# Kernel tuning notes

Measured on AMD Instinct MI355X. Metric: run time of the kernel, lower is better.

Reference implementation:

```python
import jax, jax.numpy as jnp
import numpy as np

DT = 0.001          # time step
P = 2               # geomloss p -> cost = ||x-y||^2 / 2, eps = blur**p
BLUR = 0.01
SCALING = 0.5       # eps annealing ratio per step is SCALING**P
SPARSE = 1          # sparse_sampling
N_STEPS = 24        # fixed annealing+refinement iteration count (jit-static)


def setup_inputs() -> dict:
    key = jax.random.key(0)
    k1, k2 = jax.random.split(key)
    B, S, NT, NR = 2, 4, 256, 64
    syn_data = jax.random.normal(k1, (B, S, NT, NR), jnp.float32)
    obs_data = jax.random.normal(k2, (B, S, NT, NR), jnp.float32)
    return {"syn_data": syn_data, "obs_data": obs_data}


def _softmin(eps, C, h):
    # h: [m] = log-weights + potential/eps ; C: [n, m]
    return -eps * jax.nn.logsumexp(h[None, :] - C / eps, axis=1)


def _pairwise_cost(a, b):
    # geomloss p=2 cost: squared euclidean distance / 2
    return 0.5 * jnp.sum((a[:, None, :] - b[None, :, :]) ** 2, axis=-1)


def _sinkhorn_divergence(x, y):
    # x, y: [n, 2] point clouds with uniform weights 1/n.
    # Debiased Sinkhorn divergence S = OT_eps(x,y) - 0.5 OT(x,x) - 0.5 OT(y,y)
    # computed via log-domain iterations with epsilon annealing from
    # diameter**p down to blur**p (ratio scaling**p), as in geomloss.
    n = x.shape[0]
    la = jnp.full((n,), -np.log(n), x.dtype)  # log uniform weights
    Cxy = _pairwise_cost(x, y)
    Cyx = Cxy.T
    Cxx = _pairwise_cost(x, x)
    Cyy = _pairwise_cost(y, y)

    xy = jnp.concatenate([x, y], axis=0)
    diameter = jnp.max(jnp.max(xy, axis=0) - jnp.min(xy, axis=0))
    eps0 = diameter ** P
    eps_min = jnp.asarray(BLUR ** P, x.dtype)
    ratio = SCALING ** P
    eps_list = jnp.maximum(eps0 * ratio ** jnp.arange(N_STEPS, dtype=x.dtype), eps_min)

    zeros = jnp.zeros((n,), x.dtype)

    def step(carry, eps):
        f, g, px, py = carry
        f_new = _softmin(eps, Cxy, la + g / eps)
        g_new = _softmin(eps, Cyx, la + f / eps)
        # symmetric (debiasing) potentials use damped fixed-point updates
        px_new = 0.5 * (px + _softmin(eps, Cxx, la + px / eps))
        py_new = 0.5 * (py + _softmin(eps, Cyy, la + py / eps))
        return (f_new, g_new, px_new, py_new), None

    (f, g, px, py), _ = jax.lax.scan(step, (zeros, zeros, zeros, zeros), eps_list)
    w = jnp.exp(la)  # uniform 1/n
    return jnp.sum(w * (f - px)) + jnp.sum(w * (g - py))


def reference(syn_data, obs_data):
    B, S, NT, NR = syn_data.shape
    # trace mask: drop receiver only if BOTH obs and syn traces are all-zero
    mask1 = jnp.sum(jnp.abs(obs_data), axis=2) == 0  # [B,S,NR]
    mask2 = jnp.sum(jnp.abs(syn_data), axis=2) == 0
    mask = ~(mask1 & mask2)

    t = jnp.arange(NT, dtype=syn_data.dtype)[::SPARSE] * DT  # [NTs]
    obs_tr = jnp.swapaxes(obs_data[:, :, ::SPARSE, :], 2, 3)  # [B,S,NR,NTs]
    syn_tr = jnp.swapaxes(syn_data[:, :, ::SPARSE, :], 2, 3)
    tb = jnp.broadcast_to(t, obs_tr.shape)
    obs_pts = jnp.stack([tb, obs_tr], axis=-1)  # [B,S,NR,NTs,2]
    syn_pts = jnp.stack([tb, syn_tr], axis=-1)

    nts = obs_pts.shape[3]
    flat_obs = obs_pts.reshape(B * S * NR, nts, 2)
    flat_syn = syn_pts.reshape(B * S * NR, nts, 2)
    div = jax.vmap(_sinkhorn_divergence)(flat_obs, flat_syn)  # [B*S*NR]
    div = div.reshape(B, S, NR)
    return jnp.sum(jnp.where(mask, div, jnp.zeros_like(div)), axis=(1, 2))  # [B]
```

## Files before the change

### kernel.cpp

```cpp
#include <hip/hip_runtime.h>


constexpr int   N       = 256;
constexpr int   NPROB   = 512;
constexpr int   NRDIM   = 64;
constexpr float DT_F    = 0.001f;
constexpr float EPS_MIN = 1e-4f;
constexpr int   NSTEPS  = 24;
constexpr float LOG2E   = 1.4426950408889634f;
constexpr float LN2     = 0.6931471805599453f;
constexpr int   NT      = 512;

extern "C" __global__ void __launch_bounds__(NT, 4)
sinkhorn_div_kernel(const float* __restrict__ syn,
                    const float* __restrict__ obs,
                    float* __restrict__ divs)
{
    const int p    = blockIdx.x;
    const int r    = p & (NRDIM - 1);
    const int bs   = p >> 6;
    const int tid  = threadIdx.x;
    const int row  = tid & (N - 1);
    const int pair = tid >> 8;

    __shared__ float4 ya4[2][N];
    __shared__ float4 xa4[2][N];
    __shared__ float  redA[32];

    float* yaF = (float*)ya4;
    float* xaF = (float*)xa4;

    const size_t base = (size_t)bs * N * NRDIM + r;
    const float xi = obs[base + (size_t)row * NRDIM];
    const float yi = syn[base + (size_t)row * NRDIM];
    const float ti = (float)row * DT_F;

    if (pair == 0) {
        const float2 w2 = make_float2(yi, ti);
        *(float2*)&yaF[       row * 4 + 2] = w2;
        *(float2*)&yaF[1024 + row * 4 + 2] = w2;
    } else {
        const float2 w2 = make_float2(xi, ti);
        *(float2*)&xaF[       row * 4 + 2] = w2;
        *(float2*)&xaF[1024 + row * 4 + 2] = w2;
    }

    float hi = fmaxf(xi, yi), lo = fminf(xi, yi);
    float ax = fabsf(xi),     ay = fabsf(yi);
    #pragma unroll
    for (int off = 32; off > 0; off >>= 1) {
        hi  = fmaxf(hi, __shfl_down(hi, off, 64));
        lo  = fminf(lo, __shfl_down(lo, off, 64));
        ax += __shfl_down(ax, off, 64);
        ay += __shfl_down(ay, off, 64);
    }
    const int wave = tid >> 6;
    if ((tid & 63) == 0) {
        redA[wave * 4 + 0] = hi;  redA[wave * 4 + 1] = lo;
        redA[wave * 4 + 2] = ax;  redA[wave * 4 + 3] = ay;
    }
    __syncthreads();
    float vmax = -3.4e38f, vmin = 3.4e38f, sax = 0.0f, say = 0.0f;
    #pragma unroll
    for (int w = 0; w < 8; ++w) {
        vmax = fmaxf(vmax, redA[w * 4 + 0]);
        vmin = fminf(vmin, redA[w * 4 + 1]);
        sax += redA[w * 4 + 2];
        say += redA[w * 4 + 3];
    }

    const float tspread  = 255.0f * DT_F;
    const float diameter = fmaxf(tspread, vmax - vmin);
    float eps_raw = diameter * diameter;

    const float selfx = 0.5f * (ti * ti + xi * xi);
    const float selfy = 0.5f * (ti * ti + yi * yi);
    const float la2   = -8.0f;

    const float self1 = (pair == 0) ? selfx : selfy;
    const float self2 = (pair == 0) ? selfy : selfx;
    const float cf1   = (pair == 0) ? xi : yi;
    const float cf2   = (pair == 0) ? yi : xi;

    float pot1 = 0.0f, pot2 = 0.0f;

#define EXP2(x) __builtin_amdgcn_exp2f(x)

    for (int step = 0; step < NSTEPS; ++step) {
        const float eps = fmaxf(eps_raw, EPS_MIN);
        const float inv = LOG2E / eps;
        const int   bo  = (step & 1) * 1024;

        const float h1 = fmaf(pot1 - self1, inv, la2);
        const float h2 = fmaf(pot2 - self2, inv, la2);
        if (pair == 0) {
            xaF[bo + row * 4 + 0] = h1;
            yaF[bo + row * 4 + 1] = h2;
        } else {
            yaF[bo + row * 4 + 0] = h1;
            xaF[bo + row * 4 + 1] = h2;
        }
        __syncthreads();

        const float tii = ti * inv;
        const float c1  = cf1 * inv;
        const float c2  = cf2 * inv;
        const float4* __restrict__ Hq = (pair == 0) ? &ya4[step & 1][0]
                                                    : &xa4[step & 1][0];

        float m0 = -1e9f, m1 = -1e9f, s0 = 0.0f, s1 = 0.0f;
        #pragma unroll 4
        for (int jb = 0; jb < N; jb += 8) {
            const float4 Q0 = Hq[jb + 0];
            const float4 Q1 = Hq[jb + 1];
            const float4 Q2 = Hq[jb + 2];
            const float4 Q3 = Hq[jb + 3];
            const float4 Q4 = Hq[jb + 4];
            const float4 Q5 = Hq[jb + 5];
            const float4 Q6 = Hq[jb + 6];
            const float4 Q7 = Hq[jb + 7];
            const float b0 = fmaf(c1, Q0.z, fmaf(tii, Q0.w, Q0.x));
            const float c0_ = fmaf(c2, Q0.z, fmaf(tii, Q0.w, Q0.y));
            const float b1 = fmaf(c1, Q1.z, fmaf(tii, Q1.w, Q1.x));
            const float c1_ = fmaf(c2, Q1.z, fmaf(tii, Q1.w, Q1.y));
            const float b2 = fmaf(c1, Q2.z, fmaf(tii, Q2.w, Q2.x));
            const float c2_ = fmaf(c2, Q2.z, fmaf(tii, Q2.w, Q2.y));
            const float b3 = fmaf(c1, Q3.z, fmaf(tii, Q3.w, Q3.x));
            const float c3_ = fmaf(c2, Q3.z, fmaf(tii, Q3.w, Q3.y));
            const float b4 = fmaf(c1, Q4.z, fmaf(tii, Q4.w, Q4.x));
            const float c4_ = fmaf(c2, Q4.z, fmaf(tii, Q4.w, Q4.y));
            const float b5 = fmaf(c1, Q5.z, fmaf(tii, Q5.w, Q5.x));
            const float c5_ = fmaf(c2, Q5.z, fmaf(tii, Q5.w, Q5.y));
            const float b6 = fmaf(c1, Q6.z, fmaf(tii, Q6.w, Q6.x));
            const float c6_ = fmaf(c2, Q6.z, fmaf(tii, Q6.w, Q6.y));
            const float b7 = fmaf(c1, Q7.z, fmaf(tii, Q7.w, Q7.x));
            const float c7_ = fmaf(c2, Q7.z, fmaf(tii, Q7.w, Q7.y));
            const float bt0 = fmaxf(fmaxf(b0, b1), b2);
            const float bt1 = fmaxf(fmaxf(b3, b4), b5);
            const float bt2 = fmaxf(fmaxf(b6, b7), m0);
            const float M0  = ceilf(fmaxf(fmaxf(bt0, bt1), bt2));
            const float ct0 = fmaxf(fmaxf(c0_, c1_), c2_);
            const float ct1 = fmaxf(fmaxf(c3_, c4_), c5_);
            const float ct2 = fmaxf(fmaxf(c6_, c7_), m1);
            const float M1  = ceilf(fmaxf(fmaxf(ct0, ct1), ct2));
            const float t0 =
                ((EXP2(b0 - M0) + EXP2(b1 - M0)) + (EXP2(b2 - M0) + EXP2(b3 - M0))) +
                ((EXP2(b4 - M0) + EXP2(b5 - M0)) + (EXP2(b6 - M0) + EXP2(b7 - M0)));
            const float t1 =
                ((EXP2(c0_ - M1) + EXP2(c1_ - M1)) + (EXP2(c2_ - M1) + EXP2(c3_ - M1))) +
                ((EXP2(c4_ - M1) + EXP2(c5_ - M1)) + (EXP2(c6_ - M1) + EXP2(c7_ - M1)));
            s0 = ldexpf(s0, (int)(m0 - M0)) + t0;  m0 = M0;
            s1 = ldexpf(s1, (int)(m1 - M1)) + t1;  m1 = M1;
        }

        const float el2 = eps * LN2;
        pot1 = self1 - el2 * (m0 + __builtin_amdgcn_logf(s0));
        pot2 = 0.5f * (pot2 + (self2 - el2 * (m1 + __builtin_amdgcn_logf(s1))));

        eps_raw *= 0.25f;
    }
#undef EXP2

    float contrib = pot1 - pot2;
    #pragma unroll
    for (int off = 32; off > 0; off >>= 1)
        contrib += __shfl_down(contrib, off, 64);
    __syncthreads();
    if ((tid & 63) == 0) redA[wave] = contrib;
    __syncthreads();
    if (tid == 0) {
        float total = 0.0f;
        #pragma unroll
        for (int w = 0; w < 8; ++w) total += redA[w];
        total *= (1.0f / (float)N);
        const bool masked_out = (sax == 0.0f) && (say == 0.0f);
        divs[p] = masked_out ? 0.0f : total;
    }
}

extern "C" __global__ void __launch_bounds__(256)
reduce_out_kernel(const float* __restrict__ divs, float* __restrict__ out)
{
    const int b   = blockIdx.x;
    const int tid = threadIdx.x;
    __shared__ float red[4];
    float v = divs[b * 256 + tid];
    #pragma unroll
    for (int off = 32; off > 0; off >>= 1)
        v += __shfl_down(v, off, 64);
    if ((tid & 63) == 0) red[tid >> 6] = v;
    __syncthreads();
    if (tid == 0) out[b] = red[0] + red[1] + red[2] + red[3];
}

extern "C" void kernel_launch(void* const* d_in, const int* in_sizes, int n_in,
                              void* d_out, int out_size, void* d_ws, size_t ws_size,
                              hipStream_t stream) {
    const float* syn = (const float*)d_in[0];
    const float* obs = (const float*)d_in[1];
    float* divs = (float*)d_ws;

    sinkhorn_div_kernel<<<NPROB, NT, 0, stream>>>(syn, obs, divs);
    reduce_out_kernel<<<2, 256, 0, stream>>>(divs, (float*)d_out);
}
```

Measured before the change: 589.3 us.

## Split each row's logsumexp across two half-waves with 1024-thread blocks

Doubles the block to 1024 threads so that two lanes, one in each half of a wave, cover each cost-matrix row. Each lane reduces half of the columns, and the partial (max, sum) pairs are merged with a cross-half shuffle before the potential update. This halves the serial inner-loop length per thread and adds parallelism for 512 blocks on the device. The cost is an extra shuffle-merge every step, a larger per-block footprint (launch bounds now 1024 threads with 8 waves per EU), and duplicated min/max/abs reductions in the redundant half-lanes.

```diff
diff --git a/kernel.cpp b/kernel.cpp
--- a/kernel.cpp
+++ b/kernel.cpp
@@ -9,9 +9,9 @@
 constexpr int   NSTEPS  = 24;
 constexpr float LOG2E   = 1.4426950408889634f;
 constexpr float LN2     = 0.6931471805599453f;
-constexpr int   NT      = 512;
-
-extern "C" __global__ void __launch_bounds__(NT, 4)
+constexpr int   NT      = 1024;
+
+extern "C" __global__ void __launch_bounds__(NT, 8)
 sinkhorn_div_kernel(const float* __restrict__ syn,
                     const float* __restrict__ obs,
                     float* __restrict__ divs)
@@ -20,12 +20,15 @@
     const int r    = p & (NRDIM - 1);
     const int bs   = p >> 6;
     const int tid  = threadIdx.x;
-    const int row  = tid & (N - 1);
-    const int pair = tid >> 8;
+    const int lane = tid & 63;
+    const int wave = tid >> 6;
+    const int pair = tid >> 9;
+    const int half = lane >> 5;
+    const int row  = ((wave & 7) << 5) | (lane & 31);
 
     __shared__ float4 ya4[2][N];
     __shared__ float4 xa4[2][N];
-    __shared__ float  redA[32];
+    __shared__ float  redA[64];
 
     float* yaF = (float*)ya4;
     float* xaF = (float*)xa4;
@@ -35,14 +38,16 @@
     const float yi = syn[base + (size_t)row * NRDIM];
     const float ti = (float)row * DT_F;
 
-    if (pair == 0) {
-        const float2 w2 = make_float2(yi, ti);
-        *(float2*)&yaF[       row * 4 + 2] = w2;
-        *(float2*)&yaF[1024 + row * 4 + 2] = w2;
-    } else {
-        const float2 w2 = make_float2(xi, ti);
-        *(float2*)&xaF[       row * 4 + 2] = w2;
-        *(float2*)&xaF[1024 + row * 4 + 2] = w2;
+    if (half == 0) {
+        if (pair == 0) {
+            const float2 w2 = make_float2(yi, ti);
+            *(float2*)&yaF[       row * 4 + 2] = w2;
+            *(float2*)&yaF[1024 + row * 4 + 2] = w2;
+        } else {
+            const float2 w2 = make_float2(xi, ti);
+            *(float2*)&xaF[       row * 4 + 2] = w2;
+            *(float2*)&xaF[1024 + row * 4 + 2] = w2;
+        }
     }
 
     float hi = fmaxf(xi, yi), lo = fminf(xi, yi);
@@ -54,7 +59,6 @@
         ax += __shfl_down(ax, off, 64);
         ay += __shfl_down(ay, off, 64);
     }
-    const int wave = tid >> 6;
     if ((tid & 63) == 0) {
         redA[wave * 4 + 0] = hi;  redA[wave * 4 + 1] = lo;
         redA[wave * 4 + 2] = ax;  redA[wave * 4 + 3] = ay;
@@ -62,7 +66,7 @@
     __syncthreads();
     float vmax = -3.4e38f, vmin = 3.4e38f, sax = 0.0f, say = 0.0f;
     #pragma unroll
-    for (int w = 0; w < 8; ++w) {
+    for (int w = 0; w < 16; ++w) {
         vmax = fmaxf(vmax, redA[w * 4 + 0]);
         vmin = fminf(vmin, redA[w * 4 + 1]);
         sax += redA[w * 4 + 2];
@@ -84,6 +88,8 @@
 
     float pot1 = 0.0f, pot2 = 0.0f;
 
+    const int jhalf = half << 7;
+
 #define EXP2(x) __builtin_amdgcn_exp2f(x)
 
     for (int step = 0; step < NSTEPS; ++step) {
@@ -91,14 +97,16 @@
         const float inv = LOG2E / eps;
         const int   bo  = (step & 1) * 1024;
 
-        const float h1 = fmaf(pot1 - self1, inv, la2);
-        const float h2 = fmaf(pot2 - self2, inv, la2);
-        if (pair == 0) {
-            xaF[bo + row * 4 + 0] = h1;
-            yaF[bo + row * 4 + 1] = h2;
-        } else {
-            yaF[bo + row * 4 + 0] = h1;
-            xaF[bo + row * 4 + 1] = h2;
+        if (half == 0) {
+            const float h1 = fmaf(pot1 - self1, inv, la2);
+            const float h2 = fmaf(pot2 - self2, inv, la2);
+            if (pair == 0) {
+                xaF[bo + row * 4 + 0] = h1;
+                yaF[bo + row * 4 + 1] = h2;
+            } else {
+                yaF[bo + row * 4 + 0] = h1;
+                xaF[bo + row * 4 + 1] = h2;
+            }
         }
         __syncthreads();
 
@@ -110,7 +118,8 @@
 
         float m0 = -1e9f, m1 = -1e9f, s0 = 0.0f, s1 = 0.0f;
         #pragma unroll 4
-        for (int jb = 0; jb < N; jb += 8) {
+        for (int cc = 0; cc < 128; cc += 8) {
+            const int jb = jhalf + cc;
             const float4 Q0 = Hq[jb + 0];
             const float4 Q1 = Hq[jb + 1];
             const float4 Q2 = Hq[jb + 2];
@@ -153,6 +162,27 @@
             s1 = ldexpf(s1, (int)(m1 - M1)) + t1;  m1 = M1;
         }
 
+        {
+            const float mo0 = __shfl_xor(m0, 32, 64);
+            const float so0 = __shfl_xor(s0, 32, 64);
+            const float ml  = (half == 0) ? m0 : mo0;
+            const float sl  = (half == 0) ? s0 : so0;
+            const float mh  = (half == 0) ? mo0 : m0;
+            const float sh  = (half == 0) ? so0 : s0;
+            m0 = fmaxf(ml, mh);
+            s0 = ldexpf(sl, (int)(ml - m0)) + ldexpf(sh, (int)(mh - m0));
+        }
+        {
+            const float mo1 = __shfl_xor(m1, 32, 64);
+            const float so1 = __shfl_xor(s1, 32, 64);
+            const float ml  = (half == 0) ? m1 : mo1;
+            const float sl  = (half == 0) ? s1 : so1;
+            const float mh  = (half == 0) ? mo1 : m1;
+            const float sh  = (half == 0) ? so1 : s1;
+            m1 = fmaxf(ml, mh);
+            s1 = ldexpf(sl, (int)(ml - m1)) + ldexpf(sh, (int)(mh - m1));
+        }
+
         const float el2 = eps * LN2;
         pot1 = self1 - el2 * (m0 + __builtin_amdgcn_logf(s0));
         pot2 = 0.5f * (pot2 + (self2 - el2 * (m1 + __builtin_amdgcn_logf(s1))));
@@ -161,7 +191,7 @@
     }
 #undef EXP2
 
-    float contrib = pot1 - pot2;
+    float contrib = (half == 0) ? (pot1 - pot2) : 0.0f;
     #pragma unroll
     for (int off = 32; off > 0; off >>= 1)
         contrib += __shfl_down(contrib, off, 64);
@@ -171,7 +201,7 @@
     if (tid == 0) {
         float total = 0.0f;
         #pragma unroll
-        for (int w = 0; w < 8; ++w) total += redA[w];
+        for (int w = 0; w < 16; ++w) total += redA[w];
         total *= (1.0f / (float)N);
         const bool masked_out = (sax == 0.0f) && (say == 0.0f);
         divs[p] = masked_out ? 0.0f : total;
```

Result: no change. 595.4 us (+1.0%).
